# Performance work log

Hardware: AMD Instinct MI355X
Metric: run time of the kernel (lower is better)

Reference implementation:

```python
import jax, jax.numpy as jnp
import numpy as np

CHUNK = 8           # output-channel chunk for the L1 'conv' to bound memory
EPS = 1e-5          # BatchNorm eps (torch default)
CFG = [(3, 64), (64, 128), (128, 256), (256, 256), (256, 512), (512, 512), (512, 512), (512, 512)]
POOL_AFTER = [True, True, False, True, False, True, False, True]


def adder2d(x, w, pad):
    # AdderNet layer: out[b,o,h,w] = -sum_{c,i,j} |x_patch[b,c,i,j,h,w] - w[o,c,i,j]|
    O, C, k, _ = w.shape
    patches = jax.lax.conv_general_dilated_patches(
        x, (k, k), (1, 1), [(pad, pad), (pad, pad)])  # [B, C*k*k, H, W]
    B, P, H, W = patches.shape
    wc = w.reshape(O // CHUNK, CHUNK, P)

    @jax.checkpoint
    def per_chunk(wi):  # wi: [CHUNK, P] -> [B, CHUNK, H, W]
        return -jnp.abs(patches[:, None] - wi[None, :, :, None, None]).sum(axis=2)

    out = jax.lax.map(per_chunk, wc)              # [O/CHUNK, B, CHUNK, H, W]
    return jnp.moveaxis(out, 0, 1).reshape(B, O, H, W)


def batchnorm(x, g, b):
    # training-mode BN (batch statistics), affine
    mu = jnp.mean(x, axis=(0, 2, 3), keepdims=True)
    var = jnp.mean((x - mu) ** 2, axis=(0, 2, 3), keepdims=True)
    return (x - mu) * jax.lax.rsqrt(var + EPS) * g[None, :, None, None] + b[None, :, None, None]


def maxpool2(x):
    return jax.lax.reduce_window(x, -jnp.inf, jax.lax.max, (1, 1, 2, 2), (1, 1, 2, 2), 'VALID')


def vgg11_adder_fwd(x, ws, gs, bs, wl, gl, bl):
    feats = []
    for i, w in enumerate(ws):
        x = adder2d(x, w, 1)
        x = batchnorm(x, gs[i], bs[i])
        feats.append(x)                 # features captured right after each BN
        if POOL_AFTER[i]:
            x = maxpool2(x)
        x = jax.nn.relu(x)
    x = jnp.max(x, axis=(2, 3), keepdims=True)   # adaptive_max_pool2d -> (1,1)
    x = adder2d(x, wl, 0)                        # 1x1 adder 'linear' to num_classes
    x = batchnorm(x, gl, bl)
    return x.reshape(x.shape[0], -1), feats


def setup_inputs() -> dict:
    key = jax.random.key(0)
    ks = jax.random.split(key, 16)
    d = {}
    d['x'] = jax.random.normal(ks[0], (2, 3, 96, 96), dtype=jnp.float32)
    for i, (cin, cout) in enumerate(CFG):
        std = float(np.sqrt(2.0 / (cout * 9)))  # kaiming fan_out, 3x3
        d[f'w{i+1}'] = jax.random.normal(ks[1 + i], (cout, cin, 3, 3), dtype=jnp.float32) * std
        d[f'g{i+1}'] = jnp.ones((cout,), jnp.float32)
        d[f'b{i+1}'] = jnp.zeros((cout,), jnp.float32)
    d['wl'] = jax.random.normal(ks[10], (1000, 512, 1, 1), dtype=jnp.float32) * float(np.sqrt(2.0 / 1000))
    d['gl'] = jnp.ones((1000,), jnp.float32)
    d['bl'] = jnp.zeros((1000,), jnp.float32)
    return d


def reference(x, w1, w2, w3, w4, w5, w6, w7, w8,
              g1, g2, g3, g4, g5, g6, g7, g8,
              b1, b2, b3, b4, b5, b6, b7, b8,
              wl, gl, bl):
    ws = [w1, w2, w3, w4, w5, w6, w7, w8]
    gs = [g1, g2, g3, g4, g5, g6, g7, g8]
    bs = [b1, b2, b3, b4, b5, b6, b7, b8]
    out, feats = vgg11_adder_fwd(x, ws, gs, bs, wl, gl, bl)
    return (out, *feats)
```

## Files before the change

kernel.cpp:

```cpp
#include <hip/hip_runtime.h>

#define BN_EPS 1e-5

template<int TP, int TO, int CPR>
__global__ __launch_bounds__(256) void adder_partial(
    const float* __restrict__ x, const float* __restrict__ w,
    float* __restrict__ P, int C, int H, int W, int O)
{
    constexpr int OT = 16 * TO;
    constexpr int PADOT = OT + 4;
    constexpr int NK = CPR * 9;
    constexpr int NITEMS = NK * OT;
    constexpr int ITERS = (NITEMS + 255) / 256;
    constexpr int BATCH = (ITERS < 8) ? ITERS : 8;
    __shared__ float w_s[NK][PADOT];

    const int tid = threadIdx.x;
    const int tx = tid & 15, ty = tid >> 4;
    const int o_blk = blockIdx.y * OT;
    const int tpr = W / TP;
    const int PT = 2 * H * tpr;
    const int pt = blockIdx.x * 16 + tx;
    const bool act = pt < PT;
    int b = 0, y = 0, x0 = 0;
    if (act) { int t = pt; x0 = (t % tpr) * TP; t /= tpr; y = t % H; b = t / H; }
    const int c0 = blockIdx.z * CPR;

    const float* wbase = w + ((size_t)o_blk * C + c0) * 9;
    const int c9 = C * 9;
#pragma unroll
    for (int g0 = 0; g0 < ITERS; g0 += BATCH) {
        float tmp[BATCH];
#pragma unroll
        for (int u = 0; u < BATCH; ++u) {
            int it = g0 + u;
            if (it < ITERS) {
                int idx = tid + it * 256;
                int ol = idx / NK, kk = idx - ol * NK;
                if (idx < NITEMS) tmp[u] = wbase[(size_t)ol * c9 + kk];
            }
        }
#pragma unroll
        for (int u = 0; u < BATCH; ++u) {
            int it = g0 + u;
            if (it < ITERS) {
                int idx = tid + it * 256;
                int ol = idx / NK, kk = idx - ol * NK;
                if (idx < NITEMS) w_s[kk][ol] = tmp[u];
            }
        }
    }
    __syncthreads();

    bool rv[3]; int yoff[3];
#pragma unroll
    for (int dy = 0; dy < 3; ++dy) {
        int yy = y + dy - 1;
        bool v = act && (yy >= 0) && (yy < H);
        rv[dy] = v; yoff[dy] = (v ? yy : 0) * W;
    }
    const bool lok = (x0 > 0), rok = (x0 + TP) < W;
    const int off0 = lok ? -1 : 0;
    const int offT = rok ? TP : (TP - 1);

    float acc[TO][TP] = {};

    for (int cc = 0; cc < CPR; ++cc) {
        const float* xc = x + ((size_t)(b * C + c0 + cc)) * H * W;
#pragma unroll
        for (int dy = 0; dy < 3; ++dy) {
            const float* rp = xc + yoff[dy] + x0;
            float xr[TP + 2];
            if constexpr (TP == 4) {
                float4 v = *(const float4*)rp;
                xr[1] = rv[dy] ? v.x : 0.f;
                xr[2] = rv[dy] ? v.y : 0.f;
                xr[3] = rv[dy] ? v.z : 0.f;
                xr[4] = rv[dy] ? v.w : 0.f;
                float vl = rp[off0]; xr[0]      = (rv[dy] && lok) ? vl : 0.f;
                float vr = rp[offT]; xr[TP + 1] = (rv[dy] && rok) ? vr : 0.f;
            } else {
                float2 a0 = *(const float2*)rp;
                float2 a1 = *(const float2*)(rp + 2);
                float2 a2 = *(const float2*)(rp + 4);
                xr[1] = rv[dy] ? a0.x : 0.f;
                xr[2] = rv[dy] ? a0.y : 0.f;
                xr[3] = rv[dy] ? a1.x : 0.f;
                xr[4] = rv[dy] ? a1.y : 0.f;
                xr[5] = rv[dy] ? a2.x : 0.f;
                xr[6] = rv[dy] ? a2.y : 0.f;
                float vl = rp[off0]; xr[0]      = (rv[dy] && lok) ? vl : 0.f;
                float vr = rp[offT]; xr[TP + 1] = (rv[dy] && rok) ? vr : 0.f;
            }
#pragma unroll
            for (int dx = 0; dx < 3; ++dx) {
                const float* wrow = &w_s[cc * 9 + dy * 3 + dx][ty * TO];
                float wv[TO];
                if constexpr (TO == 8) {
                    float4 wa = *(const float4*)wrow;
                    float4 wb = *(const float4*)(wrow + 4);
                    wv[0]=wa.x; wv[1]=wa.y; wv[2]=wa.z; wv[3]=wa.w;
                    wv[4]=wb.x; wv[5]=wb.y; wv[6]=wb.z; wv[7]=wb.w;
                } else if constexpr (TO == 4) {
                    float4 wa = *(const float4*)wrow;
                    wv[0]=wa.x; wv[1]=wa.y; wv[2]=wa.z; wv[3]=wa.w;
                } else {
                    float2 wa = *(const float2*)wrow;
                    wv[0]=wa.x; wv[1]=wa.y;
                }
#pragma unroll
                for (int i = 0; i < TO; i++)
#pragma unroll
                    for (int p = 0; p < TP; p++) {
                        float d;
                        asm("v_sub_f32 %1, %2, %3\n\t"
                            "v_add_f32_e64 %0, %0, |%1|"
                            : "+v"(acc[i][p]), "=&v"(d)
                            : "v"(xr[p + dx]), "v"(wv[i]));
                    }
            }
        }
    }
    if (act) {
        float* Pz = P + (size_t)blockIdx.z * ((size_t)2 * O * H * W);
        const int o0 = o_blk + ty * TO;
#pragma unroll
        for (int i = 0; i < TO; i++) {
            float* Tp = Pz + ((size_t)(b * O + (o0 + i)) * H + y) * W + x0;
            if constexpr (TP == 4) {
                *(float4*)Tp = make_float4(-acc[i][0], -acc[i][1], -acc[i][2], -acc[i][3]);
            } else {
                *(float2*)Tp       = make_float2(-acc[i][0], -acc[i][1]);
                *(float2*)(Tp + 2) = make_float2(-acc[i][2], -acc[i][3]);
                *(float2*)(Tp + 4) = make_float2(-acc[i][4], -acc[i][5]);
            }
        }
    }
}

__global__ __launch_bounds__(256) void reduce_stats(
    const float* __restrict__ P, float* __restrict__ T, double* __restrict__ dsum,
    int O, int HW, int RS)
{
    __shared__ double sh1[256];
    __shared__ double sh2[256];
    const int bc = blockIdx.x;
    const int c = bc % O;
    const int n4 = HW >> 2;
    const size_t outsz4 = (size_t)2 * O * n4;
    const float4* P4 = (const float4*)P + (size_t)bc * n4;
    float4* T4 = (float4*)T + (size_t)bc * n4;
    double a = 0.0, q = 0.0;
    for (int i4 = threadIdx.x; i4 < n4; i4 += 256) {
        float4 s0 = make_float4(0.f, 0.f, 0.f, 0.f);
        float4 s1 = make_float4(0.f, 0.f, 0.f, 0.f);
        int z = 0;
        for (; z + 1 < RS; z += 2) {
            float4 v0 = P4[(size_t)z * outsz4 + i4];
            float4 v1 = P4[(size_t)(z + 1) * outsz4 + i4];
            s0.x += v0.x; s0.y += v0.y; s0.z += v0.z; s0.w += v0.w;
            s1.x += v1.x; s1.y += v1.y; s1.z += v1.z; s1.w += v1.w;
        }
        if (z < RS) {
            float4 v = P4[(size_t)z * outsz4 + i4];
            s0.x += v.x; s0.y += v.y; s0.z += v.z; s0.w += v.w;
        }
        s0.x += s1.x; s0.y += s1.y; s0.z += s1.z; s0.w += s1.w;
        T4[i4] = s0;
        a += (double)s0.x + (double)s0.y + (double)s0.z + (double)s0.w;
        q += (double)s0.x * s0.x + (double)s0.y * s0.y
           + (double)s0.z * s0.z + (double)s0.w * s0.w;
    }
    sh1[threadIdx.x] = a; sh2[threadIdx.x] = q;
    __syncthreads();
    for (int s = 128; s > 0; s >>= 1) {
        if (threadIdx.x < s) { sh1[threadIdx.x] += sh1[threadIdx.x + s]; sh2[threadIdx.x] += sh2[threadIdx.x + s]; }
        __syncthreads();
    }
    if (threadIdx.x == 0) {
        unsafeAtomicAdd(&dsum[2 * c],     sh1[0]);
        unsafeAtomicAdd(&dsum[2 * c + 1], sh2[0]);
    }
}

__device__ __forceinline__ void bn_coef(const double* __restrict__ dsum,
                                        const float* __restrict__ g,
                                        const float* __restrict__ beta,
                                        int c, int HW, float& sc, float& sh)
{
    double n = 2.0 * (double)HW;
    double mu = dsum[2 * c] / n;
    double var = dsum[2 * c + 1] / n - mu * mu;
    double inv = 1.0 / sqrt(var + (double)BN_EPS);
    double s = (double)g[c] * inv;
    sc = (float)s;
    sh = (float)((double)beta[c] - mu * s);
}

__global__ __launch_bounds__(256) void bn_apply_pool(
    const float* __restrict__ T, const double* __restrict__ dsum,
    const float* __restrict__ g, const float* __restrict__ beta,
    float* __restrict__ feat, float* __restrict__ A, int C, int H, int W, int total)
{
    int idx = blockIdx.x * 256 + threadIdx.x;
    if (idx >= total) return;
    int Wh = W >> 1, Hh = H >> 1;
    int px = idx % Wh; int t = idx / Wh;
    int py = t % Hh; t /= Hh;
    int c = t % C; int b = t / C;
    float sc, sh;
    bn_coef(dsum, g, beta, c, H * W, sc, sh);
    size_t base = ((size_t)(b * C + c) * H + 2 * py) * W + 2 * px;
    float f0 = T[base] * sc + sh;
    float f1 = T[base + 1] * sc + sh;
    float f2 = T[base + W] * sc + sh;
    float f3 = T[base + W + 1] * sc + sh;
    feat[base] = f0; feat[base + 1] = f1; feat[base + W] = f2; feat[base + W + 1] = f3;
    A[((size_t)(b * C + c) * Hh + py) * Wh + px] = fmaxf(fmaxf(fmaxf(f0, f1), fmaxf(f2, f3)), 0.f);
}

__global__ __launch_bounds__(256) void bn_apply_np4(
    const float* __restrict__ T, const double* __restrict__ dsum,
    const float* __restrict__ g, const float* __restrict__ beta,
    float* __restrict__ feat, float* __restrict__ A, int C, int HW, int total4)
{
    int idx = blockIdx.x * 256 + threadIdx.x;
    if (idx >= total4) return;
    int e = idx * 4;
    int c = (e / HW) % C;
    float sc, sh;
    bn_coef(dsum, g, beta, c, HW, sc, sh);
    float4 t = *(const float4*)(T + e);
    float4 f = make_float4(t.x * sc + sh, t.y * sc + sh, t.z * sc + sh, t.w * sc + sh);
    *(float4*)(feat + e) = f;
    *(float4*)(A + e) = make_float4(fmaxf(f.x, 0.f), fmaxf(f.y, 0.f), fmaxf(f.z, 0.f), fmaxf(f.w, 0.f));
}

__global__ __launch_bounds__(256) void final_adder(
    const float* __restrict__ A, const float* __restrict__ wl, float* __restrict__ fo)
{
    __shared__ float xs[1024];
    for (int i = threadIdx.x; i < 1024; i += 256) {
        const float* p = A + (size_t)i * 9;
        float m = p[0];
#pragma unroll
        for (int j = 1; j < 9; j++) m = fmaxf(m, p[j]);
        xs[i] = m;
    }
    __syncthreads();
    int o = blockIdx.x * 128 + (threadIdx.x >> 1);
    int b = threadIdx.x & 1;
    if (o >= 1000) return;
    const float* wrow = wl + (size_t)o * 512;
    const float* xb = xs + b * 512;
    double s = 0.0;
    for (int c = 0; c < 512; c += 4) {
        float4 wv = *(const float4*)&wrow[c];
        s += (double)fabsf(xb[c] - wv.x) + (double)fabsf(xb[c + 1] - wv.y)
           + (double)fabsf(xb[c + 2] - wv.z) + (double)fabsf(xb[c + 3] - wv.w);
    }
    fo[b * 1000 + o] = (float)(-s);
}

__global__ __launch_bounds__(256) void final_bn(
    const float* __restrict__ fo, const float* __restrict__ gl, const float* __restrict__ bl,
    float* __restrict__ out)
{
    int o = blockIdx.x * 256 + threadIdx.x;
    if (o >= 1000) return;
    float v0 = fo[o], v1 = fo[1000 + o];
    float mu = 0.5f * (v0 + v1);
    float d = v0 - mu;
    float var = d * d;
    float iv = rsqrtf(var + (float)BN_EPS);
    float sg = iv * gl[o];
    out[o] = d * sg + bl[o];
    out[1000 + o] = -d * sg + bl[o];
}

extern "C" void kernel_launch(void* const* d_in, const int* in_sizes, int n_in,
                              void* d_out, int out_size, void* d_ws, size_t ws_size,
                              hipStream_t stream)
{
    const float* x = (const float*)d_in[0];
    const float* Wt[8]; const float* Gt[8]; const float* Bt[8];
    for (int i = 0; i < 8; i++) {
        Wt[i] = (const float*)d_in[1 + 3 * i];
        Gt[i] = (const float*)d_in[2 + 3 * i];
        Bt[i] = (const float*)d_in[3 + 3 * i];
    }
    const float* wl = (const float*)d_in[25];
    const float* gl = (const float*)d_in[26];
    const float* bl = (const float*)d_in[27];
    float* out = (float*)d_out;
    float* ws = (float*)d_ws;

    double* dsum = (double*)d_ws;
    float* T  = ws + 11008;
    float* A  = ws + 1190656;
    float* fo = ws + 1485568;
    float* P  = ws + 1487568;
    (void)ws_size;

    hipMemsetAsync(dsum, 0, 5504 * 8, stream);

    static const int Cc[8]  = {3, 64, 128, 256, 256, 512, 512, 512};
    static const int Oc[8]  = {64, 128, 256, 256, 512, 512, 512, 512};
    static const int Hc[8]  = {96, 48, 24, 24, 12, 12, 6, 6};
    static const int RSc[8] = {1, 16, 32, 32, 64, 64, 128, 128};
    static const int PLc[8] = {1, 1, 0, 1, 0, 1, 0, 1};
    static const size_t foff[8] = {2000, 1181648, 1771472, 2066384,
                                   2361296, 2508752, 2656208, 2693072};
    static const int doff[8] = {0, 128, 384, 896, 1408, 2432, 3456, 4480};

    const float* cur = x;
    for (int i = 0; i < 8; i++) {
        const int C = Cc[i], O = Oc[i], H = Hc[i], Wd = Hc[i];
        const int HW = H * Wd;
        const int rs = RSc[i];
        const int TP = (i == 0) ? 4 : 6;
        const int TO = (i == 0) ? 2 : ((i >= 6) ? 4 : 8);
        const int OT = 16 * TO;
        const int tpr = Wd / TP;
        const int PTt = 2 * H * tpr;
        dim3 grid((PTt + 15) / 16, O / OT, rs);
        if (i == 0)
            adder_partial<4, 2, 3><<<grid, 256, 0, stream>>>(cur, Wt[i], P, C, H, Wd, O);
        else if (i >= 6)
            adder_partial<6, 4, 4><<<grid, 256, 0, stream>>>(cur, Wt[i], P, C, H, Wd, O);
        else if (C / rs == 8)
            adder_partial<6, 8, 8><<<grid, 256, 0, stream>>>(cur, Wt[i], P, C, H, Wd, O);
        else
            adder_partial<6, 8, 4><<<grid, 256, 0, stream>>>(cur, Wt[i], P, C, H, Wd, O);

        double* dsum_l = dsum + doff[i];
        reduce_stats<<<2 * O, 256, 0, stream>>>(P, T, dsum_l, O, HW, rs);

        float* feat = out + foff[i];
        if (PLc[i]) {
            int total = 2 * O * (H / 2) * (Wd / 2);
            bn_apply_pool<<<(total + 255) / 256, 256, 0, stream>>>(T, dsum_l, Gt[i], Bt[i], feat, A, O, H, Wd, total);
        } else {
            int total4 = (2 * O * HW) >> 2;
            bn_apply_np4<<<(total4 + 255) / 256, 256, 0, stream>>>(T, dsum_l, Gt[i], Bt[i], feat, A, O, HW, total4);
        }
        cur = A;
    }
    final_adder<<<8, 256, 0, stream>>>(A, wl, fo);
    final_bn<<<4, 256, 0, stream>>>(fo, gl, bl, out);
}
```

Before: 373.6 us.

## Fuse split-K reduction, BN statistics and BN apply into one per-channel kernel

```diff
diff --git a/kernel.cpp b/kernel.cpp
--- a/kernel.cpp
+++ b/kernel.cpp
@@ -138,102 +138,105 @@
     }
 }
 
-__global__ __launch_bounds__(256) void reduce_stats(
-    const float* __restrict__ P, float* __restrict__ T, double* __restrict__ dsum,
-    int O, int HW, int RS)
+template<int POOL, int TLDS>
+__global__ __launch_bounds__(256) void reduce_bn_apply(
+    const float* __restrict__ P, float* __restrict__ T,
+    const float* __restrict__ g, const float* __restrict__ beta,
+    float* __restrict__ feat, float* __restrict__ A,
+    int O, int H, int W, int RS)
 {
     __shared__ double sh1[256];
     __shared__ double sh2[256];
-    const int bc = blockIdx.x;
-    const int c = bc % O;
+    __shared__ float coef[2];
+    constexpr int TBUF = TLDS ? 4608 : 4;
+    __shared__ __align__(16) float tbuf[TBUF];
+
+    const int tid = threadIdx.x;
+    const int c = blockIdx.x;
+    const int HW = H * W;
     const int n4 = HW >> 2;
     const size_t outsz4 = (size_t)2 * O * n4;
-    const float4* P4 = (const float4*)P + (size_t)bc * n4;
-    float4* T4 = (float4*)T + (size_t)bc * n4;
     double a = 0.0, q = 0.0;
-    for (int i4 = threadIdx.x; i4 < n4; i4 += 256) {
+
+    for (int idx = tid; idx < 2 * n4; idx += 256) {
+        int b = (idx >= n4) ? 1 : 0;
+        int i4 = idx - b * n4;
+        const float4* P4 = (const float4*)P + (size_t)(b * O + c) * n4 + i4;
         float4 s0 = make_float4(0.f, 0.f, 0.f, 0.f);
         float4 s1 = make_float4(0.f, 0.f, 0.f, 0.f);
         int z = 0;
         for (; z + 1 < RS; z += 2) {
-            float4 v0 = P4[(size_t)z * outsz4 + i4];
-            float4 v1 = P4[(size_t)(z + 1) * outsz4 + i4];
+            float4 v0 = P4[(size_t)z * outsz4];
+            float4 v1 = P4[(size_t)(z + 1) * outsz4];
             s0.x += v0.x; s0.y += v0.y; s0.z += v0.z; s0.w += v0.w;
             s1.x += v1.x; s1.y += v1.y; s1.z += v1.z; s1.w += v1.w;
         }
         if (z < RS) {
-            float4 v = P4[(size_t)z * outsz4 + i4];
+            float4 v = P4[(size_t)z * outsz4];
             s0.x += v.x; s0.y += v.y; s0.z += v.z; s0.w += v.w;
         }
         s0.x += s1.x; s0.y += s1.y; s0.z += s1.z; s0.w += s1.w;
-        T4[i4] = s0;
+        if constexpr (TLDS) ((float4*)tbuf)[idx] = s0;
+        else ((float4*)(T + (size_t)(b * O + c) * HW))[i4] = s0;
         a += (double)s0.x + (double)s0.y + (double)s0.z + (double)s0.w;
         q += (double)s0.x * s0.x + (double)s0.y * s0.y
            + (double)s0.z * s0.z + (double)s0.w * s0.w;
     }
-    sh1[threadIdx.x] = a; sh2[threadIdx.x] = q;
+    if constexpr (!TLDS) __threadfence_block();
+    sh1[tid] = a; sh2[tid] = q;
     __syncthreads();
     for (int s = 128; s > 0; s >>= 1) {
-        if (threadIdx.x < s) { sh1[threadIdx.x] += sh1[threadIdx.x + s]; sh2[threadIdx.x] += sh2[threadIdx.x + s]; }
+        if (tid < s) { sh1[tid] += sh1[tid + s]; sh2[tid] += sh2[tid + s]; }
         __syncthreads();
     }
-    if (threadIdx.x == 0) {
-        unsafeAtomicAdd(&dsum[2 * c],     sh1[0]);
-        unsafeAtomicAdd(&dsum[2 * c + 1], sh2[0]);
-    }
-}
-
-__device__ __forceinline__ void bn_coef(const double* __restrict__ dsum,
-                                        const float* __restrict__ g,
-                                        const float* __restrict__ beta,
-                                        int c, int HW, float& sc, float& sh)
-{
-    double n = 2.0 * (double)HW;
-    double mu = dsum[2 * c] / n;
-    double var = dsum[2 * c + 1] / n - mu * mu;
-    double inv = 1.0 / sqrt(var + (double)BN_EPS);
-    double s = (double)g[c] * inv;
-    sc = (float)s;
-    sh = (float)((double)beta[c] - mu * s);
-}
-
-__global__ __launch_bounds__(256) void bn_apply_pool(
-    const float* __restrict__ T, const double* __restrict__ dsum,
-    const float* __restrict__ g, const float* __restrict__ beta,
-    float* __restrict__ feat, float* __restrict__ A, int C, int H, int W, int total)
-{
-    int idx = blockIdx.x * 256 + threadIdx.x;
-    if (idx >= total) return;
-    int Wh = W >> 1, Hh = H >> 1;
-    int px = idx % Wh; int t = idx / Wh;
-    int py = t % Hh; t /= Hh;
-    int c = t % C; int b = t / C;
-    float sc, sh;
-    bn_coef(dsum, g, beta, c, H * W, sc, sh);
-    size_t base = ((size_t)(b * C + c) * H + 2 * py) * W + 2 * px;
-    float f0 = T[base] * sc + sh;
-    float f1 = T[base + 1] * sc + sh;
-    float f2 = T[base + W] * sc + sh;
-    float f3 = T[base + W + 1] * sc + sh;
-    feat[base] = f0; feat[base + 1] = f1; feat[base + W] = f2; feat[base + W + 1] = f3;
-    A[((size_t)(b * C + c) * Hh + py) * Wh + px] = fmaxf(fmaxf(fmaxf(f0, f1), fmaxf(f2, f3)), 0.f);
-}
-
-__global__ __launch_bounds__(256) void bn_apply_np4(
-    const float* __restrict__ T, const double* __restrict__ dsum,
-    const float* __restrict__ g, const float* __restrict__ beta,
-    float* __restrict__ feat, float* __restrict__ A, int C, int HW, int total4)
-{
-    int idx = blockIdx.x * 256 + threadIdx.x;
-    if (idx >= total4) return;
-    int e = idx * 4;
-    int c = (e / HW) % C;
-    float sc, sh;
-    bn_coef(dsum, g, beta, c, HW, sc, sh);
-    float4 t = *(const float4*)(T + e);
-    float4 f = make_float4(t.x * sc + sh, t.y * sc + sh, t.z * sc + sh, t.w * sc + sh);
-    *(float4*)(feat + e) = f;
-    *(float4*)(A + e) = make_float4(fmaxf(f.x, 0.f), fmaxf(f.y, 0.f), fmaxf(f.z, 0.f), fmaxf(f.w, 0.f));
+    if (tid == 0) {
+        double n = 2.0 * (double)HW;
+        double mu = sh1[0] / n;
+        double var = sh2[0] / n - mu * mu;
+        double inv = 1.0 / sqrt(var + (double)BN_EPS);
+        double s = (double)g[c] * inv;
+        coef[0] = (float)s;
+        coef[1] = (float)((double)beta[c] - mu * s);
+    }
+    __syncthreads();
+    const float sc = coef[0], shv = coef[1];
+
+    if constexpr (POOL) {
+        const int Wh = W >> 1, Hh = H >> 1, np = Hh * Wh;
+        for (int idx = tid; idx < 2 * np; idx += 256) {
+            int b = (idx >= np) ? 1 : 0;
+            int r = idx - b * np;
+            int py = r / Wh, px = r - py * Wh;
+            int e = (2 * py) * W + 2 * px;
+            float t0, t1, t2, t3;
+            if constexpr (TLDS) {
+                const float* tp = tbuf + b * HW + e;
+                t0 = tp[0]; t1 = tp[1]; t2 = tp[W]; t3 = tp[W + 1];
+            } else {
+                const float* tp = T + (size_t)(b * O + c) * HW + e;
+                t0 = tp[0]; t1 = tp[1]; t2 = tp[W]; t3 = tp[W + 1];
+            }
+            float f0 = t0 * sc + shv, f1 = t1 * sc + shv;
+            float f2 = t2 * sc + shv, f3 = t3 * sc + shv;
+            float* fp = feat + (size_t)(b * O + c) * HW + e;
+            fp[0] = f0; fp[1] = f1; fp[W] = f2; fp[W + 1] = f3;
+            A[((size_t)(b * O + c) * Hh + py) * Wh + px] =
+                fmaxf(fmaxf(fmaxf(f0, f1), fmaxf(f2, f3)), 0.f);
+        }
+    } else {
+        for (int idx = tid; idx < 2 * n4; idx += 256) {
+            int b = (idx >= n4) ? 1 : 0;
+            int i4 = idx - b * n4;
+            float4 t;
+            if constexpr (TLDS) t = ((float4*)tbuf)[idx];
+            else t = ((const float4*)(T + (size_t)(b * O + c) * HW))[i4];
+            float4 f = make_float4(t.x * sc + shv, t.y * sc + shv,
+                                   t.z * sc + shv, t.w * sc + shv);
+            ((float4*)(feat + (size_t)(b * O + c) * HW))[i4] = f;
+            ((float4*)(A + (size_t)(b * O + c) * HW))[i4] =
+                make_float4(fmaxf(f.x, 0.f), fmaxf(f.y, 0.f), fmaxf(f.z, 0.f), fmaxf(f.w, 0.f));
+        }
+    }
 }
 
 __global__ __launch_bounds__(256) void final_adder(
@@ -295,14 +298,11 @@
     float* out = (float*)d_out;
     float* ws = (float*)d_ws;
 
-    double* dsum = (double*)d_ws;
-    float* T  = ws + 11008;
-    float* A  = ws + 1190656;
-    float* fo = ws + 1485568;
-    float* P  = ws + 1487568;
+    float* T  = ws;
+    float* A  = ws + 1179648;
+    float* fo = ws + 1474560;
+    float* P  = ws + 1476560;
     (void)ws_size;
-
-    hipMemsetAsync(dsum, 0, 5504 * 8, stream);
 
     static const int Cc[8]  = {3, 64, 128, 256, 256, 512, 512, 512};
     static const int Oc[8]  = {64, 128, 256, 256, 512, 512, 512, 512};
@@ -311,12 +311,10 @@
     static const int PLc[8] = {1, 1, 0, 1, 0, 1, 0, 1};
     static const size_t foff[8] = {2000, 1181648, 1771472, 2066384,
                                    2361296, 2508752, 2656208, 2693072};
-    static const int doff[8] = {0, 128, 384, 896, 1408, 2432, 3456, 4480};
 
     const float* cur = x;
     for (int i = 0; i < 8; i++) {
         const int C = Cc[i], O = Oc[i], H = Hc[i], Wd = Hc[i];
-        const int HW = H * Wd;
         const int rs = RSc[i];
         const int TP = (i == 0) ? 4 : 6;
         const int TO = (i == 0) ? 2 : ((i >= 6) ? 4 : 8);
@@ -333,17 +331,13 @@
         else
             adder_partial<6, 8, 4><<<grid, 256, 0, stream>>>(cur, Wt[i], P, C, H, Wd, O);
 
-        double* dsum_l = dsum + doff[i];
-        reduce_stats<<<2 * O, 256, 0, stream>>>(P, T, dsum_l, O, HW, rs);
-
         float* feat = out + foff[i];
-        if (PLc[i]) {
-            int total = 2 * O * (H / 2) * (Wd / 2);
-            bn_apply_pool<<<(total + 255) / 256, 256, 0, stream>>>(T, dsum_l, Gt[i], Bt[i], feat, A, O, H, Wd, total);
-        } else {
-            int total4 = (2 * O * HW) >> 2;
-            bn_apply_np4<<<(total4 + 255) / 256, 256, 0, stream>>>(T, dsum_l, Gt[i], Bt[i], feat, A, O, HW, total4);
-        }
+        if (i == 0)
+            reduce_bn_apply<1, 0><<<O, 256, 0, stream>>>(P, T, Gt[i], Bt[i], feat, A, O, H, Wd, rs);
+        else if (PLc[i])
+            reduce_bn_apply<1, 1><<<O, 256, 0, stream>>>(P, T, Gt[i], Bt[i], feat, A, O, H, Wd, rs);
+        else
+            reduce_bn_apply<0, 1><<<O, 256, 0, stream>>>(P, T, Gt[i], Bt[i], feat, A, O, H, Wd, rs);
         cur = A;
     }
     final_adder<<<8, 256, 0, stream>>>(A, wl, fo);
```

New measurement: 383.5 us. +2.6%, slower.
